# Kernel optimization log

Measured on AMD Instinct MI355X. Metric: run time of the kernel, lower is better.

The kernel has to match this reference:

```python
import jax, jax.numpy as jnp
import numpy as np

N_KERNELS = 5
MUL_FACTOR = 2.0


def setup_inputs() -> dict:
    key = jax.random.key(0)
    k1, k2 = jax.random.split(key)
    x = jax.random.normal(k1, (8192, 64), dtype=jnp.float32)
    y = jax.random.normal(k2, (8192, 64), dtype=jnp.float32)
    return {"x": x, "y": y}


def reference(x, y):
    # bandwidth multipliers: mul_factor ** (arange(n) - n//2) -> [0.25,0.5,1,2,4]
    mults = MUL_FACTOR ** (jnp.arange(N_KERNELS, dtype=jnp.float32) - N_KERNELS // 2)

    z = jnp.concatenate([x, y], axis=0)  # [N, d], N = n + m
    n = x.shape[0]
    N = z.shape[0]

    # squared pairwise L2 distances: ||a||^2 + ||b||^2 - 2 a.b, clamped at 0
    sq = jnp.sum(z * z, axis=-1)  # [N]
    d2 = jnp.maximum(sq[:, None] + sq[None, :] - 2.0 * (z @ z.T), 0.0)  # [N, N]

    # data-dependent bandwidth: sum(d2) / (N^2 - N)
    bw = jnp.sum(d2) / (N * N - N)

    # multi-bandwidth RBF kernel, summed over kernels: [N, N]
    K = jnp.sum(jnp.exp(-d2[None, :, :] / (bw * mults)[:, None, None]), axis=0)

    XX = jnp.mean(K[:n, :n])
    XY = jnp.mean(K[:n, n:])
    YY = jnp.mean(K[n:, n:])
    return XX - 2.0 * XY + YY
```

## Files before the change

### kernel.cpp

```cpp
#include <hip/hip_runtime.h>
#include <hip/hip_bf16.h>

#define D 64

typedef __attribute__((ext_vector_type(8))) _Float16 half8;
typedef __attribute__((ext_vector_type(4))) float floatx4;

typedef __attribute__((address_space(1))) unsigned int gu32_t;
typedef __attribute__((address_space(3))) unsigned int lu32_t;

__global__ __launch_bounds__(256) void k_pre(const float* __restrict__ x, const float* __restrict__ y,
                                             int nx, _Float16* __restrict__ zh,
                                             float* __restrict__ sq, double* __restrict__ Tpart,
                                             float* __restrict__ Spart) {
    int tid = threadIdx.x;
    int lane = tid & 63, wid = tid >> 6;
    int t = blockIdx.x * 256 + tid;
    size_t e = (size_t)t * 8;
    int row = (int)(e >> 6);
    const float* src = (row < nx) ? (x + e) : (y + (e - (size_t)nx * D));
    float4 v0 = ((const float4*)src)[0];
    float4 v1 = ((const float4*)src)[1];
    half8 h;
    h[0]=(_Float16)v0.x; h[1]=(_Float16)v0.y; h[2]=(_Float16)v0.z; h[3]=(_Float16)v0.w;
    h[4]=(_Float16)v1.x; h[5]=(_Float16)v1.y; h[6]=(_Float16)v1.z; h[7]=(_Float16)v1.w;
    *(half8*)(zh + e) = h;
    float p = v0.x*v0.x + v0.y*v0.y + v0.z*v0.z + v0.w*v0.w
            + v1.x*v1.x + v1.y*v1.y + v1.z*v1.z + v1.w*v1.w;
    float s = p;
    s += __shfl_xor(s, 1);
    s += __shfl_xor(s, 2);
    s += __shfl_xor(s, 4);
    if ((tid & 7) == 0) sq[row] = s;

    __shared__ float colbuf[32][64];
    int rib = tid >> 3, cg = tid & 7;
    *(float4*)&colbuf[rib][cg * 8]     = v0;
    *(float4*)&colbuf[rib][cg * 8 + 4] = v1;

    double dp = (double)p;
    dp += __shfl_xor(dp, 1);
    dp += __shfl_xor(dp, 2);
    dp += __shfl_xor(dp, 4);
    dp += __shfl_xor(dp, 8);
    dp += __shfl_xor(dp, 16);
    dp += __shfl_xor(dp, 32);
    __shared__ double redw[4];
    if (lane == 0) redw[wid] = dp;
    __syncthreads();
    if (tid == 0) Tpart[blockIdx.x] = (redw[0] + redw[1]) + (redw[2] + redw[3]);

    if (tid < 64) {
        float cs = 0.f;
#pragma unroll
        for (int r2 = 0; r2 < 32; ++r2) cs += colbuf[r2][tid];
        Spart[blockIdx.x * 64 + tid] = cs;
    }
}

__global__ __launch_bounds__(256) void k_bw(const double* __restrict__ Tpart, int ntp,
                                            const float* __restrict__ Spart, int nsp,
                                            int N, float* __restrict__ cq_p) {
    int t = threadIdx.x;
    double Tp = 0.0;
    for (int b = t; b < ntp; b += 256) Tp += Tpart[b];

    int q = t >> 6, col = t & 63;
    int bpq = nsp >> 2;
    const float* sp = Spart + (size_t)(q * bpq) * 64 + col;
    float c0 = 0.f, c1 = 0.f, c2 = 0.f, c3 = 0.f;
    for (int b = 0; b < bpq; b += 4) {
        c0 += sp[(b + 0) * 64];
        c1 += sp[(b + 1) * 64];
        c2 += sp[(b + 2) * 64];
        c3 += sp[(b + 3) * 64];
    }
    __shared__ float cred[256];
    cred[t] = (c0 + c1) + (c2 + c3);

    __shared__ double red[256];
    red[t] = Tp;
    __syncthreads();
    for (int off = 128; off > 0; off >>= 1) {
        if (t < off) red[t] += red[t + off];
        __syncthreads();
    }
    double T = red[0];
    __shared__ double red2[64];
    if (t < 64) {
        float Sk = cred[t] + cred[t + 64] + cred[t + 128] + cred[t + 192];
        red2[t] = (double)Sk * (double)Sk;
    }
    __syncthreads();
    if (t == 0) {
        double S2 = 0.0;
        for (int i = 0; i < 64; ++i) S2 += red2[i];
        double sumd2 = 2.0 * (double)N * T - 2.0 * S2;
        double bw = sumd2 / ((double)N * (double)N - (double)N);
        cq_p[0] = (float)(1.4426950408889634 / (4.0 * bw));
    }
}

__global__ __launch_bounds__(256, 6) void k_mmd(const _Float16* __restrict__ zh,
                                                const float* __restrict__ sq,
                                                const float* __restrict__ cq_p,
                                                int nb, double* __restrict__ partial) {
    int bid = (nb - 1) - (int)blockIdx.x;
    int g = (int)((sqrtf(1.0f + 2.0f * (float)bid) - 1.0f) * 0.5f);
    while (2 * (g + 1) * (g + 2) <= bid) ++g;
    while (2 * g * (g + 1) > bid) --g;
    int r = bid - 2 * g * (g + 1);
    int gp1 = g + 1;
    int rig = r / gp1;
    int jc  = r - rig * gp1;
    int ib  = 4 * g + rig;

    int jstart = jc * 512;
    int jend   = (ib + 1) * 128;
    if (jend > jstart + 512) jend = jstart + 512;
    int nt = (jend - jstart) >> 5;
    int diag_j = ib * 128;

    int tid  = threadIdx.x;
    int lane = tid & 63;
    int wid  = tid >> 6;
    int i0 = ib * 128 + wid * 32;

    float cq  = cq_p[0];
    float c2q = 2.0f * cq;

    int lrow = lane & 15;
    int c2   = lane >> 4;
    int kb   = c2 * 8;

    const _Float16* ar0 = zh + (size_t)(i0 + lrow) * D + kb;
    half8 a00 = *(const half8*)(ar0);
    half8 a01 = *(const half8*)(ar0 + 32);
    half8 a10 = *(const half8*)(ar0 + 16 * D);
    half8 a11 = *(const half8*)(ar0 + 16 * D + 32);

    int irh = c2 * 4;
    float nai0[4], nai1[4];
#pragma unroll
    for (int rr = 0; rr < 4; ++rr) {
        nai0[rr] = -sq[i0 + irh + rr] * cq;
        nai1[rr] = -sq[i0 + 16 + irh + rr] * cq;
    }

    __shared__ __align__(16) _Float16 bsm[2][32 * 64];
    int srow = tid >> 3;
    int scc  = tid & 7;
    int sc   = scc ^ (srow & 7);
    const char* zbase = (const char*)zh + (size_t)jstart * 128 + srow * 128 + sc * 16;
    char* ldsw = (char*)&bsm[0][0] + wid * 1024;

    auto STAGE = [&](int buf, int tile) {
        const char* src = zbase + (size_t)tile * (32 * 128);
        __builtin_amdgcn_global_load_lds((const gu32_t*)(const void*)src,
                                         (lu32_t*)(void*)(ldsw + buf * 4096),
                                         16, 0, 0);
    };

    float acc = 0.f;

    STAGE(0, 0);
    __syncthreads();

    for (int t = 0; t < nt; ++t) {
        if (t + 1 < nt) STAGE((t + 1) & 1, t + 1);
        const char* bb = (const char*)&bsm[t & 1][0];
        int j0t = jstart + t * 32;
#pragma unroll
        for (int s = 0; s < 2; ++s) {
            int jr = s * 16 + lrow;
            int swz = jr & 7;
            half8 b0 = *(const half8*)(bb + jr * 128 + ((c2 ^ swz) * 16));
            half8 b1 = *(const half8*)(bb + jr * 128 + (((c2 + 4) ^ swz) * 16));
            float sqj = sq[j0t + s * 16 + lrow];

            floatx4 d0 = {0.f, 0.f, 0.f, 0.f};
            floatx4 d1 = {0.f, 0.f, 0.f, 0.f};
            d0 = __builtin_amdgcn_mfma_f32_16x16x32_f16(a00, b0, d0, 0, 0, 0);
            d0 = __builtin_amdgcn_mfma_f32_16x16x32_f16(a01, b1, d0, 0, 0, 0);
            d1 = __builtin_amdgcn_mfma_f32_16x16x32_f16(a10, b0, d1, 0, 0, 0);
            d1 = __builtin_amdgcn_mfma_f32_16x16x32_f16(a11, b1, d1, 0, 0, 0);

            float nbj = -sqj * cq;
            float part = 0.f;
#pragma unroll
            for (int rr = 0; rr < 4; ++rr) {
                float u0 = fminf(fmaf(d0[rr], c2q, nai0[rr] + nbj), 0.f);
                float u1 = fminf(fmaf(d1[rr], c2q, nai1[rr] + nbj), 0.f);
                float q0 = __builtin_amdgcn_exp2f(u0);
                float q1 = __builtin_amdgcn_exp2f(u1);
                float m01 = q0 * q0,   m11 = q1 * q1;
                float m02 = m01 * m01, m12 = m11 * m11;
                float m03 = m02 * m02, m13 = m12 * m12;
                float s0 = (q0 + m01) + (m02 + m03);
                float s1 = (q1 + m11) + (m12 + m13);
                part += fmaf(m03, m03, s0) + fmaf(m13, m13, s1);
            }
            float wf = ((j0t + s * 16) >= diag_j) ? 1.0f : 2.0f;
            acc = fmaf(part, wf, acc);
        }
        __syncthreads();
    }

    double wacc = (double)acc;
    wacc += __shfl_xor(wacc, 1);
    wacc += __shfl_xor(wacc, 2);
    wacc += __shfl_xor(wacc, 4);
    wacc += __shfl_xor(wacc, 8);
    wacc += __shfl_xor(wacc, 16);
    wacc += __shfl_xor(wacc, 32);
    __shared__ double redr[4];
    if (lane == 0) redr[wid] = wacc;
    __syncthreads();
    if (tid == 0) partial[bid] = (redr[0] + redr[1]) + (redr[2] + redr[3]);
}

__global__ __launch_bounds__(256) void k_final(const double* __restrict__ partial, int nb,
                                               int nxTile, int nxChunk,
                                               int nx, int ny, float* __restrict__ out) {
    int t = threadIdx.x;
    double sXX = 0.0, sXY = 0.0, sYY = 0.0;
    for (int p = t; p < nb; p += 256) {
        int g = (int)((sqrtf(1.0f + 2.0f * (float)p) - 1.0f) * 0.5f);
        while (2 * (g + 1) * (g + 2) <= p) ++g;
        while (2 * g * (g + 1) > p) --g;
        int r = p - 2 * g * (g + 1);
        int gp1 = g + 1;
        int rig = r / gp1;
        int jc  = r - rig * gp1;
        int ib  = 4 * g + rig;
        double v = partial[p];
        bool iX = ib < nxTile;
        bool jX = jc < nxChunk;
        if (iX && jX) sXX += v;
        else if (iX != jX) sXY += v;
        else sYY += v;
    }
    __shared__ double r0[256], r1[256], r2[256];
    r0[t] = sXX; r1[t] = sXY; r2[t] = sYY;
    __syncthreads();
    for (int off = 128; off > 0; off >>= 1) {
        if (t < off) {
            r0[t] += r0[t + off];
            r1[t] += r1[t + off];
            r2[t] += r2[t + off];
        }
        __syncthreads();
    }
    if (t == 0) {
        double XX = r0[0] / ((double)nx * (double)nx);
        double XY = r1[0] / (2.0 * (double)nx * (double)ny);
        double YY = r2[0] / ((double)ny * (double)ny);
        out[0] = (float)(XX - 2.0 * XY + YY);
    }
}

extern "C" void kernel_launch(void* const* d_in, const int* in_sizes, int n_in,
                              void* d_out, int out_size, void* d_ws, size_t ws_size,
                              hipStream_t stream) {
    const float* x = (const float*)d_in[0];
    const float* y = (const float*)d_in[1];
    float* out = (float*)d_out;

    int nx = in_sizes[0] / D;
    int ny = in_sizes[1] / D;
    int N  = nx + ny;

    int pre_blocks = (N * D / 8) / 256;
    int nT = N / 128;
    int ngr = nT / 4;
    int nb = 2 * ngr * (ngr + 1);
    int nxTile = nx / 128;
    int nxChunk = nx / 512;

    char* w = (char*)d_ws;
    double* Tpart   = (double*)(w + 0);
    double* partial = (double*)(w + 4096);
    float*  Spart   = (float*) (w + 20992);
    float*  sq      = (float*) (w + 152064);
    float*  cq      = (float*) (w + 217600);
    _Float16* zh    = (_Float16*)(w + 217664);

    k_pre   <<<pre_blocks, 256, 0, stream>>>(x, y, nx, zh, sq, Tpart, Spart);
    k_bw    <<<1, 256, 0, stream>>>(Tpart, pre_blocks, Spart, pre_blocks, N, cq);
    k_mmd   <<<nb, 256, 0, stream>>>(zh, sq, cq, nb, partial);
    k_final <<<1, 256, 0, stream>>>(partial, nb, nxTile, nxChunk, nx, ny, out);
}
```

Baseline: 129.0 us.

## Double j-tile to 64 rows and pack epilogue math into float2 ops

Each pipeline stage of the MMD kernel now covers 64 columns instead of 32, halving loop iterations and __syncthreads barriers and issuing two async global-to-LDS loads per stage. The exp/power-sum epilogue is rewritten with two-wide float vectors so the compiler can use packed FP32 instructions (v_pk_fma/v_pk_mul). The change doubles LDS use per block, which may reduce occupancy under the 6-waves launch bound. It also relies on tile lengths (jend-jstart) being multiples of 64, which holds given the 128-aligned bounds.

```diff
diff --git a/kernel.cpp b/kernel.cpp
--- a/kernel.cpp
+++ b/kernel.cpp
@@ -5,6 +5,7 @@
 
 typedef __attribute__((ext_vector_type(8))) _Float16 half8;
 typedef __attribute__((ext_vector_type(4))) float floatx4;
+typedef __attribute__((ext_vector_type(2))) float f32x2;
 
 typedef __attribute__((address_space(1))) unsigned int gu32_t;
 typedef __attribute__((address_space(3))) unsigned int lu32_t;
@@ -118,7 +119,7 @@
     int jstart = jc * 512;
     int jend   = (ib + 1) * 128;
     if (jend > jstart + 512) jend = jstart + 512;
-    int nt = (jend - jstart) >> 5;
+    int nt = (jend - jstart) >> 6;
     int diag_j = ib * 128;
 
     int tid  = threadIdx.x;
@@ -127,7 +128,7 @@
     int i0 = ib * 128 + wid * 32;
 
     float cq  = cq_p[0];
-    float c2q = 2.0f * cq;
+    f32x2 c2q2 = {2.0f * cq, 2.0f * cq};
 
     int lrow = lane & 15;
     int c2   = lane >> 4;
@@ -140,14 +141,13 @@
     half8 a11 = *(const half8*)(ar0 + 16 * D + 32);
 
     int irh = c2 * 4;
-    float nai0[4], nai1[4];
-#pragma unroll
-    for (int rr = 0; rr < 4; ++rr) {
-        nai0[rr] = -sq[i0 + irh + rr] * cq;
-        nai1[rr] = -sq[i0 + 16 + irh + rr] * cq;
-    }
-
-    __shared__ __align__(16) _Float16 bsm[2][32 * 64];
+    f32x2 na[4];
+    na[0] = (f32x2){-sq[i0 + irh + 0] * cq, -sq[i0 + irh + 1] * cq};
+    na[1] = (f32x2){-sq[i0 + irh + 2] * cq, -sq[i0 + irh + 3] * cq};
+    na[2] = (f32x2){-sq[i0 + 16 + irh + 0] * cq, -sq[i0 + 16 + irh + 1] * cq};
+    na[3] = (f32x2){-sq[i0 + 16 + irh + 2] * cq, -sq[i0 + 16 + irh + 3] * cq};
+
+    __shared__ __align__(16) _Float16 bsm[2][64 * 64];
     int srow = tid >> 3;
     int scc  = tid & 7;
     int sc   = scc ^ (srow & 7);
@@ -155,10 +155,12 @@
     char* ldsw = (char*)&bsm[0][0] + wid * 1024;
 
     auto STAGE = [&](int buf, int tile) {
-        const char* src = zbase + (size_t)tile * (32 * 128);
+        const char* src = zbase + (size_t)tile * (64 * 128);
+        char* dst = ldsw + buf * 8192;
         __builtin_amdgcn_global_load_lds((const gu32_t*)(const void*)src,
-                                         (lu32_t*)(void*)(ldsw + buf * 4096),
-                                         16, 0, 0);
+                                         (lu32_t*)(void*)dst, 16, 0, 0);
+        __builtin_amdgcn_global_load_lds((const gu32_t*)(const void*)(src + 32 * 128),
+                                         (lu32_t*)(void*)(dst + 4096), 16, 0, 0);
     };
 
     float acc = 0.f;
@@ -169,9 +171,9 @@
     for (int t = 0; t < nt; ++t) {
         if (t + 1 < nt) STAGE((t + 1) & 1, t + 1);
         const char* bb = (const char*)&bsm[t & 1][0];
-        int j0t = jstart + t * 32;
+        int j0t = jstart + t * 64;
 #pragma unroll
-        for (int s = 0; s < 2; ++s) {
+        for (int s = 0; s < 4; ++s) {
             int jr = s * 16 + lrow;
             int swz = jr & 7;
             half8 b0 = *(const half8*)(bb + jr * 128 + ((c2 ^ swz) * 16));
@@ -186,22 +188,30 @@
             d1 = __builtin_amdgcn_mfma_f32_16x16x32_f16(a11, b1, d1, 0, 0, 0);
 
             float nbj = -sqj * cq;
-            float part = 0.f;
+            f32x2 nb2 = {nbj, nbj};
+
+            f32x2 dd[4];
+            dd[0] = (f32x2){d0[0], d0[1]};
+            dd[1] = (f32x2){d0[2], d0[3]};
+            dd[2] = (f32x2){d1[0], d1[1]};
+            dd[3] = (f32x2){d1[2], d1[3]};
+
+            f32x2 part2 = {0.f, 0.f};
 #pragma unroll
-            for (int rr = 0; rr < 4; ++rr) {
-                float u0 = fminf(fmaf(d0[rr], c2q, nai0[rr] + nbj), 0.f);
-                float u1 = fminf(fmaf(d1[rr], c2q, nai1[rr] + nbj), 0.f);
-                float q0 = __builtin_amdgcn_exp2f(u0);
-                float q1 = __builtin_amdgcn_exp2f(u1);
-                float m01 = q0 * q0,   m11 = q1 * q1;
-                float m02 = m01 * m01, m12 = m11 * m11;
-                float m03 = m02 * m02, m13 = m12 * m12;
-                float s0 = (q0 + m01) + (m02 + m03);
-                float s1 = (q1 + m11) + (m12 + m13);
-                part += fmaf(m03, m03, s0) + fmaf(m13, m13, s1);
+            for (int pk = 0; pk < 4; ++pk) {
+                f32x2 u = dd[pk] * c2q2 + (na[pk] + nb2);
+                u.x = fminf(u.x, 0.f);
+                u.y = fminf(u.y, 0.f);
+                f32x2 q;
+                q.x = __builtin_amdgcn_exp2f(u.x);
+                q.y = __builtin_amdgcn_exp2f(u.y);
+                f32x2 m1 = q * q;
+                f32x2 m2 = m1 * m1;
+                f32x2 m3 = m2 * m2;
+                part2 += ((q + m1) + (m2 + m3)) + m3 * m3;
             }
             float wf = ((j0t + s * 16) >= diag_j) ? 1.0f : 2.0f;
-            acc = fmaf(part, wf, acc);
+            acc = fmaf(part2.x + part2.y, wf, acc);
         }
         __syncthreads();
     }
```

New measurement: 127.2 us. Within noise of the previous version (-1.4%).
